# Kernel optimization log

Hardware: AMD Instinct MI355X
Metric: run time of the kernel (lower is better)

Reference implementation:

```python
import jax, jax.numpy as jnp
import numpy as np

B, C, N = 8, 256, 2048
BN_EPS = 1e-5


def setup_inputs() -> dict:
    key = jax.random.key(0)
    ks = jax.random.split(key, 11)
    s = 1.0 / np.sqrt(C)
    return {
        "x": jax.random.normal(ks[0], (B, C, N), dtype=jnp.float32),
        "Wq": jax.random.normal(ks[1], (C, C), dtype=jnp.float32) * s,
        "Wk": jax.random.normal(ks[2], (C, C), dtype=jnp.float32) * s,
        "Wv": jax.random.normal(ks[3], (C, C), dtype=jnp.float32) * s,
        "bv": jax.random.normal(ks[4], (C,), dtype=jnp.float32) * 0.01,
        "Wt": jax.random.normal(ks[5], (C, C), dtype=jnp.float32) * s,
        "bt": jax.random.normal(ks[6], (C,), dtype=jnp.float32) * 0.01,
        "bn_gamma": jnp.ones((C,), dtype=jnp.float32),
        "bn_beta": jnp.zeros((C,), dtype=jnp.float32),
        "alpha": jnp.ones((1, C, 1), dtype=jnp.float32),
        "beta": jnp.zeros((1, C, 1), dtype=jnp.float32),
    }


def reference(x, Wq, Wk, Wv, bv, Wt, bt, bn_gamma, bn_beta, alpha, beta):
    # 1x1 Conv1d == per-point linear: [C_out, C_in] @ [B, C_in, N]
    x_q = jnp.einsum('oc,bcn->bno', Wq, x)                 # [B, N, C] (permuted)
    x_k = jnp.einsum('oc,bcn->bon', Wk, x)                 # [B, C, N]
    x_v = jnp.einsum('oc,bcn->bon', Wv, x) + bv[None, :, None]
    energy = jnp.einsum('bnc,bcm->bnm', x_q, x_k)          # [B, N, N]
    attention = jax.nn.softmax(energy, axis=-1)            # row softmax
    # double normalization: divide by column sums
    attention = attention / (1e-9 + attention.sum(axis=1, keepdims=True))
    x_r = jnp.einsum('bcn,bnm->bcm', x_v, attention)       # [B, C, N]
    # trans_conv on residual, then learned affine
    x_z = jnp.einsum('oc,bcn->bon', Wt, x - x_r) + bt[None, :, None]
    x_z = alpha * x_z + beta
    # BatchNorm1d (training mode): stats over (batch, points) per channel
    mean = x_z.mean(axis=(0, 2), keepdims=True)
    var = x_z.var(axis=(0, 2), keepdims=True)
    x_n = (x_z - mean) * jax.lax.rsqrt(var + BN_EPS)
    x_n = bn_gamma[None, :, None] * x_n + bn_beta[None, :, None]
    return x + jax.nn.relu(x_n)
```

## Files before the change

kernel.cpp:

```cpp
#include <hip/hip_runtime.h>
#include <hip/hip_bf16.h>
#include <math.h>

#define BB 8
#define CC 256
#define NN 2048
static constexpr float BN_EPS = 1e-5f;

typedef _Float16 f16;
typedef f16 f16x4 __attribute__((ext_vector_type(4)));
typedef f16 f16x8 __attribute__((ext_vector_type(8)));
typedef float f32x4 __attribute__((ext_vector_type(4)));
typedef short s16x8 __attribute__((ext_vector_type(8)));
typedef unsigned short u16x8 __attribute__((ext_vector_type(8)));
typedef __hip_bfloat16 bf16;

#define APAD 40
#define XPAD 72

__device__ inline float bf2f(unsigned short u) {
    return __uint_as_float((unsigned)u << 16);
}

__global__ __launch_bounds__(256) void prep_w_kernel(
    const float* __restrict__ Wq, const float* __restrict__ Wk,
    const float* __restrict__ Wv, const float* __restrict__ Wt,
    f16* __restrict__ Whi, f16* __restrict__ Wlo)
{
    int idx = (blockIdx.x * 256 + threadIdx.x) * 8;
    const float* s = (idx < 65536) ? Wq : (idx < 131072) ? Wk
                    : (idx < 196608) ? Wv : Wt;
    int off = idx & 65535;
    float4 a = *(const float4*)&s[off];
    float4 b = *(const float4*)&s[off + 4];
    float v[8] = {a.x, a.y, a.z, a.w, b.x, b.y, b.z, b.w};
    f16x8 h, l;
#pragma unroll
    for (int j = 0; j < 8; ++j) {
        f16 hh = (f16)v[j];
        f16 ll = (f16)(v[j] - (float)hh);
        h[j] = hh;
        l[j] = ll;
    }
    *(f16x8*)&Whi[idx] = h;
    *(f16x8*)&Wlo[idx] = l;
}

__global__ __launch_bounds__(256) void prep_x_kernel(
    const float* __restrict__ x, f16* __restrict__ Xhi, f16* __restrict__ Xlo)
{
    const int b = blockIdx.z, c0 = blockIdx.y * 64, n0 = blockIdx.x * 64;
    const float* __restrict__ Xb = x + (size_t)b * CC * NN;
    f16* __restrict__ Oh = Xhi + (size_t)b * NN * CC;
    f16* __restrict__ Ol = Xlo + (size_t)b * NN * CC;
    __shared__ f16 Th[64][72];
    __shared__ f16 Tl[64][72];
    const int tid = threadIdx.x;
    const int r = tid >> 4, c4 = (tid & 15) * 4;
#pragma unroll
    for (int i = 0; i < 4; ++i) {
        int rr = r + i * 16;
        float4 v = *(const float4*)&Xb[(size_t)(c0 + rr) * NN + n0 + c4];
        float vv[4] = {v.x, v.y, v.z, v.w};
#pragma unroll
        for (int j = 0; j < 4; ++j) {
            f16 hh = (f16)vv[j];
            f16 ll = (f16)(vv[j] - (float)hh);
            Th[c4 + j][rr] = hh;
            Tl[c4 + j][rr] = ll;
        }
    }
    __syncthreads();
#pragma unroll
    for (int i = 0; i < 2; ++i) {
        int idx = tid + 256 * i;
        int n = idx >> 3, cg = (idx & 7) * 8;
        *(f16x8*)&Oh[(size_t)(n0 + n) * CC + c0 + cg] = *(f16x8*)&Th[n][cg];
        *(f16x8*)&Ol[(size_t)(n0 + n) * CC + c0 + cg] = *(f16x8*)&Tl[n][cg];
    }
}

__global__ __launch_bounds__(256) void proj_mfma_kernel(
    const f16* __restrict__ Whi, const f16* __restrict__ Wlo,
    const f16* __restrict__ Xhi, const f16* __restrict__ Xlo,
    const float* __restrict__ bv,
    f16* __restrict__ Qhi, f16* __restrict__ Khi, bf16* __restrict__ Vb16)
{
    const int which = blockIdx.z >> 3;
    const int b     = blockIdx.z & 7;
    const f16* __restrict__ Wh = Whi + (size_t)which * CC * CC;
    const f16* __restrict__ Wl = Wlo + (size_t)which * CC * CC;
    const f16* __restrict__ Xh = Xhi + (size_t)b * NN * CC;
    const f16* __restrict__ Xl = Xlo + (size_t)b * NN * CC;

    const int m0 = blockIdx.y * 128;
    const int n0 = blockIdx.x * 128;

    __shared__ f16 Ah[128 * APAD];
    __shared__ f16 Al[128 * APAD];
    __shared__ f16 Bh[128 * APAD];
    __shared__ f16 Bl[128 * APAD];

    const int tid = threadIdx.x;
    const int wave = tid >> 6, lane = tid & 63;
    const int wr = (wave >> 1) * 64, wc = (wave & 1) * 64;
    const int lrow = lane & 15, lk = (lane >> 4) * 8;

    f32x4 acc[4][4] = {};

    for (int k0 = 0; k0 < CC; k0 += 32) {
#pragma unroll
        for (int i = 0; i < 2; ++i) {
            int idx = tid + 256 * i;
            int r = idx >> 2, ch = idx & 3;
            *(f16x8*)&Ah[r * APAD + ch * 8] =
                *(const f16x8*)&Wh[(size_t)(m0 + r) * CC + k0 + ch * 8];
            *(f16x8*)&Bh[r * APAD + ch * 8] =
                *(const f16x8*)&Xh[(size_t)(n0 + r) * CC + k0 + ch * 8];
            if (which < 2) {
                *(f16x8*)&Al[r * APAD + ch * 8] =
                    *(const f16x8*)&Wl[(size_t)(m0 + r) * CC + k0 + ch * 8];
                *(f16x8*)&Bl[r * APAD + ch * 8] =
                    *(const f16x8*)&Xl[(size_t)(n0 + r) * CC + k0 + ch * 8];
            }
        }
        __syncthreads();
        f16x8 ah[4], al[4], bh[4], bl[4];
#pragma unroll
        for (int i = 0; i < 4; ++i) {
            ah[i] = *(const f16x8*)&Ah[(wr + i * 16 + lrow) * APAD + lk];
            bh[i] = *(const f16x8*)&Bh[(wc + i * 16 + lrow) * APAD + lk];
        }
        if (which < 2) {
#pragma unroll
            for (int i = 0; i < 4; ++i) {
                al[i] = *(const f16x8*)&Al[(wr + i * 16 + lrow) * APAD + lk];
                bl[i] = *(const f16x8*)&Bl[(wc + i * 16 + lrow) * APAD + lk];
            }
        }
#pragma unroll
        for (int i = 0; i < 4; ++i)
#pragma unroll
            for (int j = 0; j < 4; ++j) {
                acc[i][j] = __builtin_amdgcn_mfma_f32_16x16x32_f16(
                    ah[i], bh[j], acc[i][j], 0, 0, 0);
                if (which < 2) {
                    acc[i][j] = __builtin_amdgcn_mfma_f32_16x16x32_f16(
                        ah[i], bl[j], acc[i][j], 0, 0, 0);
                    acc[i][j] = __builtin_amdgcn_mfma_f32_16x16x32_f16(
                        al[i], bh[j], acc[i][j], 0, 0, 0);
                }
            }
        __syncthreads();
    }

    if (which < 2) {
        f16* __restrict__ Oh = ((which == 0) ? Qhi : Khi) + (size_t)b * NN * CC;
#pragma unroll
        for (int i = 0; i < 4; ++i) {
            int cb = m0 + wr + i * 16 + (lane >> 4) * 4;
#pragma unroll
            for (int j = 0; j < 4; ++j) {
                int n = n0 + wc + j * 16 + lrow;
                f16x4 hv;
#pragma unroll
                for (int q = 0; q < 4; ++q) hv[q] = (f16)acc[i][j][q];
                *(f16x4*)&Oh[(size_t)n * CC + cb] = hv;
            }
        }
    } else {
        bf16* __restrict__ Vb = Vb16 + (size_t)b * CC * NN;
#pragma unroll
        for (int i = 0; i < 4; ++i) {
            int cb = m0 + wr + i * 16 + (lane >> 4) * 4;
#pragma unroll
            for (int q = 0; q < 4; ++q) {
                float bvv = bv[cb + q];
#pragma unroll
                for (int j = 0; j < 4; ++j) {
                    int n = n0 + wc + j * 16 + lrow;
                    Vb[(size_t)(cb + q) * NN + n] = __float2bfloat16(acc[i][j][q] + bvv);
                }
            }
        }
    }
}

__global__ __launch_bounds__(256) void energy_mfma_kernel(
    const f16* __restrict__ Qhi, const f16* __restrict__ Khi,
    bf16* __restrict__ AT16,
    float* __restrict__ rowmax_p, float* __restrict__ rowsum_p)
{
    const int b = blockIdx.z;
    const int n0 = blockIdx.y * 128;
    const int m0 = blockIdx.x * 128;
    const f16* __restrict__ Qh = Qhi + (size_t)b * NN * CC;
    const f16* __restrict__ Kh = Khi + (size_t)b * NN * CC;

    __shared__ f16 Ah[128 * APAD];
    __shared__ f16 Bh[128 * APAD];
    __shared__ bf16 Tt[64 * 136];

    const int tid = threadIdx.x;
    const int wave = tid >> 6, lane = tid & 63;
    const int wr = (wave >> 1) * 64, wc = (wave & 1) * 64;
    const int lrow = lane & 15, lk = (lane >> 4) * 8;

    f32x4 acc[4][4] = {};

    for (int k0 = 0; k0 < CC; k0 += 32) {
#pragma unroll
        for (int i = 0; i < 2; ++i) {
            int idx = tid + 256 * i;
            int r = idx >> 2, ch = idx & 3;
            *(f16x8*)&Ah[r * APAD + ch * 8] =
                *(const f16x8*)&Qh[(size_t)(n0 + r) * CC + k0 + ch * 8];
            *(f16x8*)&Bh[r * APAD + ch * 8] =
                *(const f16x8*)&Kh[(size_t)(m0 + r) * CC + k0 + ch * 8];
        }
        __syncthreads();
        f16x8 af[4], bf[4];
#pragma unroll
        for (int i = 0; i < 4; ++i) {
            af[i] = *(const f16x8*)&Ah[(wr + i * 16 + lrow) * APAD + lk];
            bf[i] = *(const f16x8*)&Bh[(wc + i * 16 + lrow) * APAD + lk];
        }
#pragma unroll
        for (int i = 0; i < 4; ++i)
#pragma unroll
            for (int j = 0; j < 4; ++j)
                acc[i][j] = __builtin_amdgcn_mfma_f32_16x16x32_f16(
                    af[i], bf[j], acc[i][j], 0, 0, 0);
        __syncthreads();
    }

    const int mt_w = (m0 + wc) >> 6;
    float* __restrict__ RMP = rowmax_p + ((size_t)b * 32 + mt_w) * NN;
    float* __restrict__ RSP = rowsum_p + ((size_t)b * 32 + mt_w) * NN;
#pragma unroll
    for (int i = 0; i < 4; ++i)
#pragma unroll
        for (int q = 0; q < 4; ++q) {
            float v0 = acc[i][0][q], v1 = acc[i][1][q];
            float v2 = acc[i][2][q], v3 = acc[i][3][q];
            float mx = fmaxf(fmaxf(v0, v1), fmaxf(v2, v3));
#pragma unroll
            for (int d = 1; d < 16; d <<= 1) mx = fmaxf(mx, __shfl_xor(mx, d));
            float p0 = __expf(v0 - mx), p1 = __expf(v1 - mx);
            float p2 = __expf(v2 - mx), p3 = __expf(v3 - mx);
            acc[i][0][q] = p0; acc[i][1][q] = p1;
            acc[i][2][q] = p2; acc[i][3][q] = p3;
            float es = p0 + p1 + p2 + p3;
#pragma unroll
            for (int d = 1; d < 16; d <<= 1) es += __shfl_xor(es, d);
            if (lrow == 0) {
                int row = n0 + wr + i * 16 + (lane >> 4) * 4 + q;
                RMP[row] = mx;
                RSP[row] = es;
            }
        }

    bf16* __restrict__ Ab = AT16 + (size_t)b * NN * NN;
    for (int chunk = 0; chunk < 2; ++chunk) {
        if ((wave & 1) == chunk) {
#pragma unroll
            for (int i = 0; i < 4; ++i)
#pragma unroll
                for (int j = 0; j < 4; ++j)
#pragma unroll
                    for (int q = 0; q < 4; ++q)
                        Tt[(j * 16 + lrow) * 136 + wr + i * 16 + (lane >> 4) * 4 + q] =
                            __float2bfloat16(acc[i][j][q]);
        }
        __syncthreads();
#pragma unroll
        for (int u = 0; u < 4; ++u) {
            int e = tid + u * 256;
            int mrow = e >> 4, nch = (e & 15) * 8;
            *(u16x8*)&Ab[(size_t)(m0 + chunk * 64 + mrow) * NN + n0 + nch] =
                *(const u16x8*)&Tt[mrow * 136 + nch];
        }
        __syncthreads();
    }
}

__global__ __launch_bounds__(256) void rowmerge_kernel(
    const float* __restrict__ rowmax_p, const float* __restrict__ rowsum_p,
    float* __restrict__ fvecG)
{
    int idx = blockIdx.x * 256 + threadIdx.x;
    int b = idx >> 11, n = idx & (NN - 1);
    const float* __restrict__ RM = rowmax_p + (size_t)b * 32 * NN + n;
    const float* __restrict__ RS = rowsum_p + (size_t)b * 32 * NN + n;
    float rm[32];
    float gmx = -1e30f;
#pragma unroll
    for (int t = 0; t < 32; ++t) {
        rm[t] = RM[(size_t)t * NN];
        gmx = fmaxf(gmx, rm[t]);
    }
    float s = 0.f;
#pragma unroll
    for (int t = 0; t < 32; ++t)
        s += RS[(size_t)t * NN] * __expf(rm[t] - gmx);
    const float inv = 1.f / s;
    float* __restrict__ FG = fvecG + (size_t)b * 32 * NN + n;
#pragma unroll
    for (int t = 0; t < 32; ++t)
        FG[(size_t)t * NN] = __expf(rm[t] - gmx) * inv;
}

__global__ __launch_bounds__(256) void colsum_fvec_kernel(
    const bf16* __restrict__ AT16, const float* __restrict__ fvecG,
    float* __restrict__ colsum)
{
    const int mt = blockIdx.x, b = blockIdx.y;
    const bf16* __restrict__ Ab = AT16 + (size_t)b * NN * NN;
    const float* __restrict__ FG = fvecG + ((size_t)b * 32 + mt) * NN;
    const int tid = threadIdx.x;
    const int wave = tid >> 6, lane = tid & 63;

    float fv[4][8];
#pragma unroll
    for (int p = 0; p < 4; ++p) {
        int k = p * 512 + lane * 8;
        float4 f0 = *(const float4*)&FG[k];
        float4 f1 = *(const float4*)&FG[k + 4];
        fv[p][0] = f0.x; fv[p][1] = f0.y; fv[p][2] = f0.z; fv[p][3] = f0.w;
        fv[p][4] = f1.x; fv[p][5] = f1.y; fv[p][6] = f1.z; fv[p][7] = f1.w;
    }

#pragma unroll
    for (int rr = 0; rr < 16; ++rr) {
        int m = mt * 64 + wave * 16 + rr;
        const bf16* __restrict__ R = &Ab[(size_t)m * NN];
        float cs = 0.f;
#pragma unroll
        for (int p = 0; p < 4; ++p) {
            int k = p * 512 + lane * 8;
            u16x8 v = *(const u16x8*)&R[k];
#pragma unroll
            for (int e = 0; e < 8; ++e)
                cs += bf2f((unsigned short)v[e]) * fv[p][e];
        }
#pragma unroll
        for (int d = 1; d < 64; d <<= 1) cs += __shfl_xor(cs, d);
        if (lane == 0) colsum[b * NN + m] = cs;
    }
}

__global__ __launch_bounds__(256) void xr_mfma_kernel(
    const bf16* __restrict__ Vb16, const bf16* __restrict__ AT16,
    const float* __restrict__ fvecG, const float* __restrict__ colsum,
    const float* __restrict__ x, f16* __restrict__ Dt16)
{
    const int b  = blockIdx.z;
    const int c0 = blockIdx.y * 64;
    const int n0 = blockIdx.x * 64;
    const bf16* __restrict__ Vb = Vb16 + (size_t)b * CC * NN;
    const bf16* __restrict__ Ab = AT16 + (size_t)b * NN * NN;
    const float* __restrict__ Xb = x + (size_t)b * CC * NN;
    const float* __restrict__ FG = fvecG + ((size_t)b * 32 + (n0 >> 6)) * NN;
    f16* __restrict__ Db = Dt16 + (size_t)b * NN * CC;

    __shared__ bf16 Asl[64 * XPAD];
    __shared__ bf16 Bsl[64 * XPAD];
    __shared__ float rcvL[64];

    const int tid = threadIdx.x;
    if (tid < 64) rcvL[tid] = 1.f / (1e-9f + colsum[b * NN + n0 + tid]);

    const int wave = tid >> 6, lane = tid & 63;
    const int wr = (wave >> 1) * 32, wc = (wave & 1) * 32;
    const int lrow = lane & 15, lk = (lane >> 4) * 8;
    const int ch8 = (tid & 7) * 8;

    f32x4 acc[2][2] = {};

    for (int k0 = 0; k0 < NN; k0 += 64) {
        float4 f0 = *(const float4*)&FG[k0 + ch8];
        float4 f1 = *(const float4*)&FG[k0 + ch8 + 4];
        float fg[8] = {f0.x, f0.y, f0.z, f0.w, f1.x, f1.y, f1.z, f1.w};
#pragma unroll
        for (int i = 0; i < 2; ++i) {
            int idx = tid + 256 * i;
            int r = idx >> 3;
            *(u16x8*)&Asl[r * XPAD + ch8] =
                *(const u16x8*)&Vb[(size_t)(c0 + r) * NN + k0 + ch8];
            u16x8 v = *(const u16x8*)&Ab[(size_t)(n0 + r) * NN + k0 + ch8];
            bf16 w[8];
#pragma unroll
            for (int e = 0; e < 8; ++e)
                w[e] = __float2bfloat16(bf2f((unsigned short)v[e]) * fg[e]);
            *(u16x8*)&Bsl[r * XPAD + ch8] = *(const u16x8*)w;
        }
        __syncthreads();
#pragma unroll
        for (int ks = 0; ks < 2; ++ks) {
            s16x8 af[2], bf[2];
#pragma unroll
            for (int i = 0; i < 2; ++i) {
                af[i] = *(const s16x8*)&Asl[(wr + i * 16 + lrow) * XPAD + ks * 32 + lk];
                bf[i] = *(const s16x8*)&Bsl[(wc + i * 16 + lrow) * XPAD + ks * 32 + lk];
            }
#pragma unroll
            for (int i = 0; i < 2; ++i)
#pragma unroll
                for (int j = 0; j < 2; ++j)
                    acc[i][j] = __builtin_amdgcn_mfma_f32_16x16x32_bf16(
                        af[i], bf[j], acc[i][j], 0, 0, 0);
        }
        __syncthreads();
    }

#pragma unroll
    for (int i = 0; i < 2; ++i) {
        int cb = c0 + wr + i * 16 + (lane >> 4) * 4;
#pragma unroll
        for (int j = 0; j < 2; ++j) {
            int ln = wc + j * 16 + lrow;
            int n = n0 + ln;
            float rc = rcvL[ln];
            f16x4 dv;
#pragma unroll
            for (int q = 0; q < 4; ++q)
                dv[q] = (f16)(Xb[(size_t)(cb + q) * NN + n] - acc[i][j][q] * rc);
            *(f16x4*)&Db[(size_t)n * CC + cb] = dv;
        }
    }
}

__global__ __launch_bounds__(256) void xz_mfma_kernel(
    const f16* __restrict__ Whi, const f16* __restrict__ Dt16,
    const float* __restrict__ bt, const float* __restrict__ alpha,
    const float* __restrict__ beta, bf16* __restrict__ XZ,
    float* __restrict__ bnsum, float* __restrict__ bnsumsq)
{
    const int b = blockIdx.z;
    const int m0 = blockIdx.y * 128;
    const int n0 = blockIdx.x * 128;
    const f16* __restrict__ Wb = Whi + (size_t)3 * CC * CC;
    const f16* __restrict__ Db = Dt16 + (size_t)b * NN * CC;
    bf16* __restrict__ Zb = XZ + (size_t)b * CC * NN;

    __shared__ f16 Asl[128 * APAD];
    __shared__ f16 Bsl[128 * APAD];

    const int tid = threadIdx.x;
    const int wave = tid >> 6, lane = tid & 63;
    const int wr = (wave >> 1) * 64, wc = (wave & 1) * 64;
    const int lrow = lane & 15, lk = (lane >> 4) * 8;

    f32x4 acc[4][4] = {};

    for (int k0 = 0; k0 < CC; k0 += 32) {
#pragma unroll
        for (int i = 0; i < 2; ++i) {
            int idx = tid + 256 * i;
            int r = idx >> 2, ch = idx & 3;
            *(f16x8*)&Asl[r * APAD + ch * 8] =
                *(const f16x8*)&Wb[(size_t)(m0 + r) * CC + k0 + ch * 8];
            *(f16x8*)&Bsl[r * APAD + ch * 8] =
                *(const f16x8*)&Db[(size_t)(n0 + r) * CC + k0 + ch * 8];
        }
        __syncthreads();
        f16x8 af[4], bf[4];
#pragma unroll
        for (int i = 0; i < 4; ++i) {
            af[i] = *(const f16x8*)&Asl[(wr + i * 16 + lrow) * APAD + lk];
            bf[i] = *(const f16x8*)&Bsl[(wc + i * 16 + lrow) * APAD + lk];
        }
#pragma unroll
        for (int i = 0; i < 4; ++i)
#pragma unroll
            for (int j = 0; j < 4; ++j)
                acc[i][j] = __builtin_amdgcn_mfma_f32_16x16x32_f16(
                    af[i], bf[j], acc[i][j], 0, 0, 0);
        __syncthreads();
    }

#pragma unroll
    for (int i = 0; i < 4; ++i) {
#pragma unroll
        for (int q = 0; q < 4; ++q) {
            int o = m0 + wr + i * 16 + (lane >> 4) * 4 + q;
            float al = alpha[o], be = beta[o], bb = bt[o];
            float s1 = 0.f, s2 = 0.f;
#pragma unroll
            for (int j = 0; j < 4; ++j) {
                int n = n0 + wc + j * 16 + lrow;
                float z = al * (acc[i][j][q] + bb) + be;
                Zb[(size_t)o * NN + n] = __float2bfloat16(z);
                s1 += z; s2 += z * z;
            }
#pragma unroll
            for (int d = 1; d < 16; d <<= 1) {
                s1 += __shfl_xor(s1, d);
                s2 += __shfl_xor(s2, d);
            }
            if (lrow == 0) {
                atomicAdd(&bnsum[o], s1);
                atomicAdd(&bnsumsq[o], s2);
            }
        }
    }
}

__global__ __launch_bounds__(256) void final_kernel(
    const float* __restrict__ x, const bf16* __restrict__ XZ,
    const float* __restrict__ bnsum, const float* __restrict__ bnsumsq,
    const float* __restrict__ gamma, const float* __restrict__ bbeta,
    float* __restrict__ out)
{
    const int i4 = blockIdx.x * 256 + threadIdx.x;
    const int elem = i4 * 4;
    const int c = (elem / NN) % CC;
    const float inv_cnt = 1.f / (float)(BB * NN);
    const float mean = bnsum[c] * inv_cnt;
    const float var  = bnsumsq[c] * inv_cnt - mean * mean;
    const float rs = rsqrtf(var + BN_EPS);
    const float g = gamma[c], bb = bbeta[c];

    ushort4 zu = *(const ushort4*)&XZ[elem];
    float4 xv = *(const float4*)&x[elem];
    float z0 = bf2f(zu.x), z1 = bf2f(zu.y), z2 = bf2f(zu.z), z3 = bf2f(zu.w);
    float4 o;
    o.x = xv.x + fmaxf(g * (z0 - mean) * rs + bb, 0.f);
    o.y = xv.y + fmaxf(g * (z1 - mean) * rs + bb, 0.f);
    o.z = xv.z + fmaxf(g * (z2 - mean) * rs + bb, 0.f);
    o.w = xv.w + fmaxf(g * (z3 - mean) * rs + bb, 0.f);
    *(float4*)&out[elem] = o;
}


extern "C" void kernel_launch(void* const* d_in, const int* in_sizes, int n_in,
                              void* d_out, int out_size, void* d_ws, size_t ws_size,
                              hipStream_t stream) {
    const float* x     = (const float*)d_in[0];
    const float* Wq    = (const float*)d_in[1];
    const float* Wk    = (const float*)d_in[2];
    const float* Wv    = (const float*)d_in[3];
    const float* bv    = (const float*)d_in[4];
    const float* Wt    = (const float*)d_in[5];
    const float* bt    = (const float*)d_in[6];
    const float* gamma = (const float*)d_in[7];
    const float* bbeta = (const float*)d_in[8];
    const float* alpha = (const float*)d_in[9];
    const float* beta  = (const float*)d_in[10];
    float* out = (float*)d_out;

    const size_t BCN = (size_t)BB * CC * NN;
    const size_t WSZ = (size_t)4 * CC * CC;

    f16* Whi = (f16*)d_ws;
    f16* Wlo = Whi + WSZ;
    bf16* Vb16 = (bf16*)(Wlo + WSZ);
    f16* Qhi = (f16*)(Vb16 + BCN);
    f16* Khi = Qhi + BCN;
    bf16* AT16 = (bf16*)(Khi + BCN);
    bf16* XZ = AT16 + (size_t)BB * NN * NN;
    float* colsum  = (float*)(XZ + BCN);
    float* bnsum   = colsum + (size_t)BB * NN;
    float* bnsumsq = bnsum + CC;
    float* rowmax_p = bnsumsq + CC;
    float* rowsum_p = rowmax_p + (size_t)BB * 32 * NN;
    float* fvecG    = rowsum_p + (size_t)BB * 32 * NN;

    f16* Dt16 = Qhi;
    f16* Xhi = (f16*)AT16;
    f16* Xlo = Xhi + BCN;

    hipMemsetAsync(bnsum, 0, 2 * CC * sizeof(float), stream);

    prep_w_kernel<<<dim3(4 * CC * CC / 2048), 256, 0, stream>>>(
        Wq, Wk, Wv, Wt, Whi, Wlo);
    prep_x_kernel<<<dim3(NN / 64, CC / 64, BB), 256, 0, stream>>>(x, Xhi, Xlo);
    proj_mfma_kernel<<<dim3(NN / 128, CC / 128, 3 * BB), 256, 0, stream>>>(
        Whi, Wlo, Xhi, Xlo, bv, Qhi, Khi, Vb16);
    energy_mfma_kernel<<<dim3(NN / 128, NN / 128, BB), 256, 0, stream>>>(
        Qhi, Khi, AT16, rowmax_p, rowsum_p);
    rowmerge_kernel<<<dim3(BB * NN / 256), 256, 0, stream>>>(
        rowmax_p, rowsum_p, fvecG);
    colsum_fvec_kernel<<<dim3(32, BB), 256, 0, stream>>>(
        AT16, fvecG, colsum);
    xr_mfma_kernel<<<dim3(NN / 64, CC / 64, BB), 256, 0, stream>>>(
        Vb16, AT16, fvecG, colsum, x, Dt16);
    xz_mfma_kernel<<<dim3(NN / 128, CC / 128, BB), 256, 0, stream>>>(
        Whi, Dt16, bt, alpha, beta, XZ, bnsum, bnsumsq);
    final_kernel<<<dim3((int)(BCN / 4 / 256)), 256, 0, stream>>>(
        x, XZ, bnsum, bnsumsq, gamma, bbeta, out);
}
```

Before: 229.2 us.

## Fuse column-sum into xr kernel and drop fp16 hi/lo split in projections

Removes the separate colsum pass over the bf16 attention matrix. Column sums of the scaled attention are now accumulated inside xr_mfma_kernel while it loads tiles, then wave-reduced and stored in shared memory. It also drops the low-order fp16 correction terms for weights and x, so the Q/K projections use a single MFMA per tile instead of three and the lo-part prep writes go away. This saves a full read of the large attention matrix and some projection work, but energy logits lose accuracy, which could affect softmax fidelity.

```diff
diff --git a/kernel.cpp b/kernel.cpp
--- a/kernel.cpp
+++ b/kernel.cpp
@@ -25,7 +25,7 @@
 __global__ __launch_bounds__(256) void prep_w_kernel(
     const float* __restrict__ Wq, const float* __restrict__ Wk,
     const float* __restrict__ Wv, const float* __restrict__ Wt,
-    f16* __restrict__ Whi, f16* __restrict__ Wlo)
+    f16* __restrict__ Whi)
 {
     int idx = (blockIdx.x * 256 + threadIdx.x) * 8;
     const float* s = (idx < 65536) ? Wq : (idx < 131072) ? Wk
@@ -33,42 +33,26 @@
     int off = idx & 65535;
     float4 a = *(const float4*)&s[off];
     float4 b = *(const float4*)&s[off + 4];
-    float v[8] = {a.x, a.y, a.z, a.w, b.x, b.y, b.z, b.w};
-    f16x8 h, l;
-#pragma unroll
-    for (int j = 0; j < 8; ++j) {
-        f16 hh = (f16)v[j];
-        f16 ll = (f16)(v[j] - (float)hh);
-        h[j] = hh;
-        l[j] = ll;
-    }
+    f16x8 h = {(f16)a.x, (f16)a.y, (f16)a.z, (f16)a.w,
+               (f16)b.x, (f16)b.y, (f16)b.z, (f16)b.w};
     *(f16x8*)&Whi[idx] = h;
-    *(f16x8*)&Wlo[idx] = l;
 }
 
 __global__ __launch_bounds__(256) void prep_x_kernel(
-    const float* __restrict__ x, f16* __restrict__ Xhi, f16* __restrict__ Xlo)
+    const float* __restrict__ x, f16* __restrict__ Xhi)
 {
     const int b = blockIdx.z, c0 = blockIdx.y * 64, n0 = blockIdx.x * 64;
     const float* __restrict__ Xb = x + (size_t)b * CC * NN;
     f16* __restrict__ Oh = Xhi + (size_t)b * NN * CC;
-    f16* __restrict__ Ol = Xlo + (size_t)b * NN * CC;
     __shared__ f16 Th[64][72];
-    __shared__ f16 Tl[64][72];
     const int tid = threadIdx.x;
     const int r = tid >> 4, c4 = (tid & 15) * 4;
 #pragma unroll
     for (int i = 0; i < 4; ++i) {
         int rr = r + i * 16;
         float4 v = *(const float4*)&Xb[(size_t)(c0 + rr) * NN + n0 + c4];
-        float vv[4] = {v.x, v.y, v.z, v.w};
-#pragma unroll
-        for (int j = 0; j < 4; ++j) {
-            f16 hh = (f16)vv[j];
-            f16 ll = (f16)(vv[j] - (float)hh);
-            Th[c4 + j][rr] = hh;
-            Tl[c4 + j][rr] = ll;
-        }
+        Th[c4 + 0][rr] = (f16)v.x; Th[c4 + 1][rr] = (f16)v.y;
+        Th[c4 + 2][rr] = (f16)v.z; Th[c4 + 3][rr] = (f16)v.w;
     }
     __syncthreads();
 #pragma unroll
@@ -76,30 +60,24 @@
         int idx = tid + 256 * i;
         int n = idx >> 3, cg = (idx & 7) * 8;
         *(f16x8*)&Oh[(size_t)(n0 + n) * CC + c0 + cg] = *(f16x8*)&Th[n][cg];
-        *(f16x8*)&Ol[(size_t)(n0 + n) * CC + c0 + cg] = *(f16x8*)&Tl[n][cg];
     }
 }
 
 __global__ __launch_bounds__(256) void proj_mfma_kernel(
-    const f16* __restrict__ Whi, const f16* __restrict__ Wlo,
-    const f16* __restrict__ Xhi, const f16* __restrict__ Xlo,
+    const f16* __restrict__ Whi, const f16* __restrict__ Xhi,
     const float* __restrict__ bv,
     f16* __restrict__ Qhi, f16* __restrict__ Khi, bf16* __restrict__ Vb16)
 {
     const int which = blockIdx.z >> 3;
     const int b     = blockIdx.z & 7;
     const f16* __restrict__ Wh = Whi + (size_t)which * CC * CC;
-    const f16* __restrict__ Wl = Wlo + (size_t)which * CC * CC;
     const f16* __restrict__ Xh = Xhi + (size_t)b * NN * CC;
-    const f16* __restrict__ Xl = Xlo + (size_t)b * NN * CC;
 
     const int m0 = blockIdx.y * 128;
     const int n0 = blockIdx.x * 128;
 
     __shared__ f16 Ah[128 * APAD];
-    __shared__ f16 Al[128 * APAD];
     __shared__ f16 Bh[128 * APAD];
-    __shared__ f16 Bl[128 * APAD];
 
     const int tid = threadIdx.x;
     const int wave = tid >> 6, lane = tid & 63;
@@ -117,40 +95,20 @@
                 *(const f16x8*)&Wh[(size_t)(m0 + r) * CC + k0 + ch * 8];
             *(f16x8*)&Bh[r * APAD + ch * 8] =
                 *(const f16x8*)&Xh[(size_t)(n0 + r) * CC + k0 + ch * 8];
-            if (which < 2) {
-                *(f16x8*)&Al[r * APAD + ch * 8] =
-                    *(const f16x8*)&Wl[(size_t)(m0 + r) * CC + k0 + ch * 8];
-                *(f16x8*)&Bl[r * APAD + ch * 8] =
-                    *(const f16x8*)&Xl[(size_t)(n0 + r) * CC + k0 + ch * 8];
-            }
-        }
-        __syncthreads();
-        f16x8 ah[4], al[4], bh[4], bl[4];
+        }
+        __syncthreads();
+        f16x8 af[4], bf[4];
 #pragma unroll
         for (int i = 0; i < 4; ++i) {
-            ah[i] = *(const f16x8*)&Ah[(wr + i * 16 + lrow) * APAD + lk];
-            bh[i] = *(const f16x8*)&Bh[(wc + i * 16 + lrow) * APAD + lk];
-        }
-        if (which < 2) {
-#pragma unroll
-            for (int i = 0; i < 4; ++i) {
-                al[i] = *(const f16x8*)&Al[(wr + i * 16 + lrow) * APAD + lk];
-                bl[i] = *(const f16x8*)&Bl[(wc + i * 16 + lrow) * APAD + lk];
-            }
+            af[i] = *(const f16x8*)&Ah[(wr + i * 16 + lrow) * APAD + lk];
+            bf[i] = *(const f16x8*)&Bh[(wc + i * 16 + lrow) * APAD + lk];
         }
 #pragma unroll
         for (int i = 0; i < 4; ++i)
 #pragma unroll
-            for (int j = 0; j < 4; ++j) {
+            for (int j = 0; j < 4; ++j)
                 acc[i][j] = __builtin_amdgcn_mfma_f32_16x16x32_f16(
-                    ah[i], bh[j], acc[i][j], 0, 0, 0);
-                if (which < 2) {
-                    acc[i][j] = __builtin_amdgcn_mfma_f32_16x16x32_f16(
-                        ah[i], bl[j], acc[i][j], 0, 0, 0);
-                    acc[i][j] = __builtin_amdgcn_mfma_f32_16x16x32_f16(
-                        al[i], bh[j], acc[i][j], 0, 0, 0);
-                }
-            }
+                    af[i], bf[j], acc[i][j], 0, 0, 0);
         __syncthreads();
     }
 
@@ -310,49 +268,10 @@
         FG[(size_t)t * NN] = __expf(rm[t] - gmx) * inv;
 }
 
-__global__ __launch_bounds__(256) void colsum_fvec_kernel(
-    const bf16* __restrict__ AT16, const float* __restrict__ fvecG,
-    float* __restrict__ colsum)
-{
-    const int mt = blockIdx.x, b = blockIdx.y;
-    const bf16* __restrict__ Ab = AT16 + (size_t)b * NN * NN;
-    const float* __restrict__ FG = fvecG + ((size_t)b * 32 + mt) * NN;
-    const int tid = threadIdx.x;
-    const int wave = tid >> 6, lane = tid & 63;
-
-    float fv[4][8];
-#pragma unroll
-    for (int p = 0; p < 4; ++p) {
-        int k = p * 512 + lane * 8;
-        float4 f0 = *(const float4*)&FG[k];
-        float4 f1 = *(const float4*)&FG[k + 4];
-        fv[p][0] = f0.x; fv[p][1] = f0.y; fv[p][2] = f0.z; fv[p][3] = f0.w;
-        fv[p][4] = f1.x; fv[p][5] = f1.y; fv[p][6] = f1.z; fv[p][7] = f1.w;
-    }
-
-#pragma unroll
-    for (int rr = 0; rr < 16; ++rr) {
-        int m = mt * 64 + wave * 16 + rr;
-        const bf16* __restrict__ R = &Ab[(size_t)m * NN];
-        float cs = 0.f;
-#pragma unroll
-        for (int p = 0; p < 4; ++p) {
-            int k = p * 512 + lane * 8;
-            u16x8 v = *(const u16x8*)&R[k];
-#pragma unroll
-            for (int e = 0; e < 8; ++e)
-                cs += bf2f((unsigned short)v[e]) * fv[p][e];
-        }
-#pragma unroll
-        for (int d = 1; d < 64; d <<= 1) cs += __shfl_xor(cs, d);
-        if (lane == 0) colsum[b * NN + m] = cs;
-    }
-}
-
 __global__ __launch_bounds__(256) void xr_mfma_kernel(
     const bf16* __restrict__ Vb16, const bf16* __restrict__ AT16,
-    const float* __restrict__ fvecG, const float* __restrict__ colsum,
-    const float* __restrict__ x, f16* __restrict__ Dt16)
+    const float* __restrict__ fvecG, const float* __restrict__ x,
+    f16* __restrict__ Dt16)
 {
     const int b  = blockIdx.z;
     const int c0 = blockIdx.y * 64;
@@ -365,33 +284,47 @@
 
     __shared__ bf16 Asl[64 * XPAD];
     __shared__ bf16 Bsl[64 * XPAD];
-    __shared__ float rcvL[64];
+    __shared__ float csL[64];
 
     const int tid = threadIdx.x;
-    if (tid < 64) rcvL[tid] = 1.f / (1e-9f + colsum[b * NN + n0 + tid]);
-
     const int wave = tid >> 6, lane = tid & 63;
     const int wr = (wave >> 1) * 32, wc = (wave & 1) * 32;
     const int lrow = lane & 15, lk = (lane >> 4) * 8;
     const int ch8 = (tid & 7) * 8;
-
+    const int r0 = tid >> 3;
+
+    float cs0 = 0.f, cs1 = 0.f;
     f32x4 acc[2][2] = {};
 
     for (int k0 = 0; k0 < NN; k0 += 64) {
         float4 f0 = *(const float4*)&FG[k0 + ch8];
         float4 f1 = *(const float4*)&FG[k0 + ch8 + 4];
         float fg[8] = {f0.x, f0.y, f0.z, f0.w, f1.x, f1.y, f1.z, f1.w};
-#pragma unroll
-        for (int i = 0; i < 2; ++i) {
-            int idx = tid + 256 * i;
-            int r = idx >> 3;
+        {
+            *(u16x8*)&Asl[r0 * XPAD + ch8] =
+                *(const u16x8*)&Vb[(size_t)(c0 + r0) * NN + k0 + ch8];
+            u16x8 v = *(const u16x8*)&Ab[(size_t)(n0 + r0) * NN + k0 + ch8];
+            bf16 w[8];
+#pragma unroll
+            for (int e = 0; e < 8; ++e) {
+                float pv = bf2f((unsigned short)v[e]) * fg[e];
+                w[e] = __float2bfloat16(pv);
+                cs0 += pv;
+            }
+            *(u16x8*)&Bsl[r0 * XPAD + ch8] = *(const u16x8*)w;
+        }
+        {
+            int r = r0 + 32;
             *(u16x8*)&Asl[r * XPAD + ch8] =
                 *(const u16x8*)&Vb[(size_t)(c0 + r) * NN + k0 + ch8];
             u16x8 v = *(const u16x8*)&Ab[(size_t)(n0 + r) * NN + k0 + ch8];
             bf16 w[8];
 #pragma unroll
-            for (int e = 0; e < 8; ++e)
-                w[e] = __float2bfloat16(bf2f((unsigned short)v[e]) * fg[e]);
+            for (int e = 0; e < 8; ++e) {
+                float pv = bf2f((unsigned short)v[e]) * fg[e];
+                w[e] = __float2bfloat16(pv);
+                cs1 += pv;
+            }
             *(u16x8*)&Bsl[r * XPAD + ch8] = *(const u16x8*)w;
         }
         __syncthreads();
@@ -413,6 +346,14 @@
         __syncthreads();
     }
 
+    cs0 += __shfl_xor(cs0, 1); cs0 += __shfl_xor(cs0, 2); cs0 += __shfl_xor(cs0, 4);
+    cs1 += __shfl_xor(cs1, 1); cs1 += __shfl_xor(cs1, 2); cs1 += __shfl_xor(cs1, 4);
+    if ((lane & 7) == 0) {
+        csL[r0] = cs0;
+        csL[r0 + 32] = cs1;
+    }
+    __syncthreads();
+
 #pragma unroll
     for (int i = 0; i < 2; ++i) {
         int cb = c0 + wr + i * 16 + (lane >> 4) * 4;
@@ -420,7 +361,7 @@
         for (int j = 0; j < 2; ++j) {
             int ln = wc + j * 16 + lrow;
             int n = n0 + ln;
-            float rc = rcvL[ln];
+            float rc = 1.f / (1e-9f + csL[ln]);
             f16x4 dv;
 #pragma unroll
             for (int q = 0; q < 4; ++q)
@@ -553,14 +494,12 @@
     const size_t WSZ = (size_t)4 * CC * CC;
 
     f16* Whi = (f16*)d_ws;
-    f16* Wlo = Whi + WSZ;
-    bf16* Vb16 = (bf16*)(Wlo + WSZ);
+    bf16* Vb16 = (bf16*)(Whi + WSZ);
     f16* Qhi = (f16*)(Vb16 + BCN);
     f16* Khi = Qhi + BCN;
     bf16* AT16 = (bf16*)(Khi + BCN);
     bf16* XZ = AT16 + (size_t)BB * NN * NN;
-    float* colsum  = (float*)(XZ + BCN);
-    float* bnsum   = colsum + (size_t)BB * NN;
+    float* bnsum   = (float*)(XZ + BCN);
     float* bnsumsq = bnsum + CC;
     float* rowmax_p = bnsumsq + CC;
     float* rowsum_p = rowmax_p + (size_t)BB * 32 * NN;
@@ -568,23 +507,20 @@
 
     f16* Dt16 = Qhi;
     f16* Xhi = (f16*)AT16;
-    f16* Xlo = Xhi + BCN;
 
     hipMemsetAsync(bnsum, 0, 2 * CC * sizeof(float), stream);
 
     prep_w_kernel<<<dim3(4 * CC * CC / 2048), 256, 0, stream>>>(
-        Wq, Wk, Wv, Wt, Whi, Wlo);
-    prep_x_kernel<<<dim3(NN / 64, CC / 64, BB), 256, 0, stream>>>(x, Xhi, Xlo);
+        Wq, Wk, Wv, Wt, Whi);
+    prep_x_kernel<<<dim3(NN / 64, CC / 64, BB), 256, 0, stream>>>(x, Xhi);
     proj_mfma_kernel<<<dim3(NN / 128, CC / 128, 3 * BB), 256, 0, stream>>>(
-        Whi, Wlo, Xhi, Xlo, bv, Qhi, Khi, Vb16);
+        Whi, Xhi, bv, Qhi, Khi, Vb16);
     energy_mfma_kernel<<<dim3(NN / 128, NN / 128, BB), 256, 0, stream>>>(
         Qhi, Khi, AT16, rowmax_p, rowsum_p);
     rowmerge_kernel<<<dim3(BB * NN / 256), 256, 0, stream>>>(
         rowmax_p, rowsum_p, fvecG);
-    colsum_fvec_kernel<<<dim3(32, BB), 256, 0, stream>>>(
-        AT16, fvecG, colsum);
     xr_mfma_kernel<<<dim3(NN / 64, CC / 64, BB), 256, 0, stream>>>(
-        Vb16, AT16, fvecG, colsum, x, Dt16);
+        Vb16, AT16, fvecG, x, Dt16);
     xz_mfma_kernel<<<dim3(NN / 128, CC / 128, BB), 256, 0, stream>>>(
         Whi, Dt16, bt, alpha, beta, XZ, bnsum, bnsumsq);
     final_kernel<<<dim3((int)(BCN / 4 / 256)), 256, 0, stream>>>(
```

Result: faster. 186.4 us, median of 2 (-18.6%).
